# Performance work log

Measured on AMD Instinct MI355X. Metric: run time of the kernel, lower is better.

The kernel has to match this reference:

```python
import jax, jax.numpy as jnp
import numpy as np

TRUNC = (24, 24, 24)
OUT = (32, 32, 32)


def setup_inputs() -> dict:
    key = jax.random.key(0)
    x = jax.random.normal(key, (8, 32, 48, 48, 48), dtype=jnp.float32)
    return {"x": x}


def reference(x):
    # "DCT" as implemented in the source: real part of an ortho-normalized 3D FFT
    x_dct = jnp.real(jnp.fft.fftn(x, axes=(2, 3, 4), norm='ortho'))
    # crop to low-frequency corner, zero-pad up to output_size
    x_crop = x_dct[:, :, :TRUNC[0], :TRUNC[1], :TRUNC[2]]
    pad = ((0, 0), (0, 0),
           (0, OUT[0] - TRUNC[0]),
           (0, OUT[1] - TRUNC[1]),
           (0, OUT[2] - TRUNC[2]))
    x_pad = jnp.pad(x_crop, pad)
    # inverse transform on the output_size grid, keep real part
    x_idct = jnp.real(jnp.fft.ifftn(x_pad, axes=(2, 3, 4), norm='ortho'))
    return x_idct
```

## Files before the change

kernel.cpp:

```cpp
#include <hip/hip_runtime.h>
#include <math.h>


#define TWO_PI_48 0.13089969389957470f
#define TWO_PI_32 0.19634954084936207f
#define NORM_F    1.6611664e-05f

typedef _Float16 half8  __attribute__((ext_vector_type(8)));
typedef _Float16 half4v __attribute__((ext_vector_type(4)));
typedef float    f32x4  __attribute__((ext_vector_type(4)));

__device__ _Float16 T1frag[2][3][2][64][8];
__device__ _Float16 T2frag[2][3][2][64][8];
__device__ __align__(16) _Float16 TK2frag[2][4][3][64][8];
__device__ __align__(16) _Float16 MB2frag[2][4][2][64][8];
__device__ __align__(16) _Float16 TB3frag[2][2][2][64][8];

__device__ int g_twdone = 0;

__global__ void k_init_tw() {
  if (g_twdone) return;
  const int idx = blockIdx.x * 256 + threadIdx.x;
  if (idx < 3072) {
    const int j  = idx & 7;
    const int l  = (idx >> 3) & 63;
    const int ks = (idx >> 9) & 1;
    const int t  = idx >> 10;
    const int k  = ks * 32 + (l >> 4) * 8 + j;
    {
      const int m = t * 16 + (l & 15);
      float v = 0.f;
      if (k < 48) {
        const float a = (float)(((m % 24) * k) % 48) * TWO_PI_48;
        v = (m < 24) ? cosf(a) : -sinf(a);
      }
      const _Float16 h = (_Float16)v;
      T1frag[0][t][ks][l][j] = h;
      T1frag[1][t][ks][l][j] = (_Float16)(v - (float)h);
    }
    {
      const int c = t * 16 + (l & 15);
      float v = 0.f;
      if (k < 48) {
        const float a = (float)(((c % 24) * k) % 48) * TWO_PI_48;
        v = (c < 24) ? cosf(a) : sinf(a);
      }
      const _Float16 h = (_Float16)v;
      T2frag[0][t][ks][l][j] = h;
      T2frag[1][t][ks][l][j] = (_Float16)(v - (float)h);
    }
  } else if (idx < 3072 + 6144) {
    const int local = idx - 3072;
    const int j = local & 7, l = (local >> 3) & 63;
    const int rest = local >> 9;
    const int ks = rest % 3, mt = rest / 3;
    const int m   = mt * 16 + (l & 15);
    const int kap = ks * 32 + (l >> 4) * 8 + j;
    const int n1  = kap % 48;
    const bool isVi = kap >= 48;
    const int m1  = m & 31;
    const bool isWi = m >= 32;
    float acc = 0.f;
    for (int k1 = 0; k1 < 24; ++k1) {
      float s32v, c32v, s48v, c48v;
      sincosf((float)((k1 * m1) % 32) * TWO_PI_32, &s32v, &c32v);
      sincosf((float)((k1 * n1) % 48) * TWO_PI_48, &s48v, &c48v);
      acc = fmaf(isWi ? s32v : c32v, isVi ? s48v : c48v, acc);
    }
    const _Float16 h = (_Float16)acc;
    TK2frag[0][mt][ks][l][j] = h;
    TK2frag[1][mt][ks][l][j] = (_Float16)(acc - (float)h);
  } else if (idx < 3072 + 6144 + 4096) {
    const int local = idx - (3072 + 6144);
    const int j = local & 7, l = (local >> 3) & 63;
    const int rest = local >> 9;
    const int ks = rest & 1, mt = rest >> 1;
    const int m   = mt * 16 + (l & 15);
    const int kap = ks * 32 + (l >> 4) * 8 + j;
    float v = 0.f;
    if (kap < 48) {
      const int k2 = kap % 24;
      const int m2 = m & 31;
      float s, c;
      sincosf((float)((k2 * m2) % 32) * TWO_PI_32, &s, &c);
      if (m < 32) v = (kap < 24) ? c : -s;
      else        v = (kap < 24) ? s :  c;
    }
    const _Float16 h = (_Float16)v;
    MB2frag[0][mt][ks][l][j] = h;
    MB2frag[1][mt][ks][l][j] = (_Float16)(v - (float)h);
  } else if (idx < 15360) {
    const int local = idx - (3072 + 6144 + 4096);
    const int j = local & 7, l = (local >> 3) & 63;
    const int rest = local >> 9;
    const int ks = rest & 1, nt = rest >> 1;
    const int m3  = nt * 16 + (l & 15);
    const int kap = ks * 32 + (l >> 4) * 8 + j;
    float v = 0.f;
    if (kap < 48) {
      const int k3 = kap % 24;
      float s, c;
      sincosf((float)((k3 * m3) % 32) * TWO_PI_32, &s, &c);
      v = (kap < 24) ? c : -s;
    }
    const _Float16 h = (_Float16)v;
    TB3frag[0][nt][ks][l][j] = h;
    TB3frag[1][nt][ks][l][j] = (_Float16)(v - (float)h);
  }
}

__device__ inline void split8(const float* qf, half8& h, half8& lo) {
#pragma unroll
  for (int j = 0; j < 8; ++j) {
    const _Float16 hh = (_Float16)qf[j];
    h[j]  = hh;
    lo[j] = (_Float16)(qf[j] - (float)hh);
  }
}

__global__ __launch_bounds__(64) void k1_waveslab(const float* __restrict__ x,
                                                  float2* __restrict__ V) {
  const int n1   = blockIdx.x;
  const int bc   = blockIdx.y;
  const int lane = threadIdx.x;

  __shared__ __align__(16) unsigned char arena[13824];
  _Float16* Uh = (_Float16*)arena;
  _Float16* Ul = (_Float16*)(arena + 6912);
  float*    D2 = (float*)arena;

  const int c16  = lane & 15;
  const int kgrp = lane >> 4;
  const int kb   = kgrp * 8;

  const float* xs = x + (size_t)(bc * 48 + n1) * 2304;

  float4 xf[3][2][2];
  {
    const int k1i = 32 + kb;
#pragma unroll
    for (int nt = 0; nt < 3; ++nt) {
      const int c = nt * 16 + c16;
      const float4* p0 = (const float4*)(xs + c * 48 + kb);
      xf[nt][0][0] = p0[0]; xf[nt][0][1] = p0[1];
      if (k1i < 48) {
        const float4* p1 = (const float4*)(xs + c * 48 + k1i);
        xf[nt][1][0] = p1[0]; xf[nt][1][1] = p1[1];
      } else {
        xf[nt][1][0] = make_float4(0.f, 0.f, 0.f, 0.f);
        xf[nt][1][1] = make_float4(0.f, 0.f, 0.f, 0.f);
      }
    }
  }

  half8 t1h[3][2], t1l[3][2];
#pragma unroll
  for (int mt = 0; mt < 3; ++mt)
#pragma unroll
    for (int ks = 0; ks < 2; ++ks) {
      t1h[mt][ks] = *(const half8*)&T1frag[0][mt][ks][lane][0];
      t1l[mt][ks] = *(const half8*)&T1frag[1][mt][ks][lane][0];
    }

#pragma unroll
  for (int p = 0; p < 3; ++p) {
    const int i = lane + 64 * p;
    const int which = i / 48, r = i % 48;
    _Float16* base = (which & 2) ? Ul : Uh;
    *(half8*)&base[r * 72 + 48 + (which & 1) * 8] = (half8){};
  }

#pragma unroll
  for (int nt = 0; nt < 3; ++nt) {
    f32x4 acc0 = {}, acc1 = {}, acc2 = {};
#pragma unroll
    for (int ks = 0; ks < 2; ++ks) {
      const float4 qa = xf[nt][ks][0];
      const float4 qb = xf[nt][ks][1];
      const float qf[8] = {qa.x, qa.y, qa.z, qa.w, qb.x, qb.y, qb.z, qb.w};
      half8 bh, bl;
      split8(qf, bh, bl);
#pragma unroll
      for (int mt = 0; mt < 3; ++mt) {
        f32x4& acc = (mt == 0) ? acc0 : (mt == 1) ? acc1 : acc2;
        acc = __builtin_amdgcn_mfma_f32_16x16x32_f16(t1h[mt][ks], bh, acc, 0, 0, 0);
        acc = __builtin_amdgcn_mfma_f32_16x16x32_f16(t1h[mt][ks], bl, acc, 0, 0, 0);
        acc = __builtin_amdgcn_mfma_f32_16x16x32_f16(t1l[mt][ks], bh, acc, 0, 0, 0);
      }
    }

    {
      const int cc = nt * 16 + c16;
#pragma unroll
      for (int mt = 0; mt < 3; ++mt) {
        const int r0 = mt * 16 + kgrp * 4;
        const f32x4 acc = (mt == 0) ? acc0 : (mt == 1) ? acc1 : acc2;
#pragma unroll
        for (int r = 0; r < 4; ++r) {
          const float v = acc[r];
          const _Float16 h = (_Float16)v;
          Uh[(r0 + r) * 72 + cc] = h;
          Ul[(r0 + r) * 72 + cc] = (_Float16)(v - (float)h);
        }
      }
    }
  }

  half8 t2h[3][2], t2l[3][2];
#pragma unroll
  for (int mt = 0; mt < 3; ++mt)
#pragma unroll
    for (int ks = 0; ks < 2; ++ks) {
      t2h[mt][ks] = *(const half8*)&T2frag[0][mt][ks][lane][0];
      t2l[mt][ks] = *(const half8*)&T2frag[1][mt][ks][lane][0];
    }

  f32x4 a2[3][3] = {};
#pragma unroll
  for (int ks = 0; ks < 2; ++ks) {
#pragma unroll
    for (int mt = 0; mt < 3; ++mt) {
      const half8 ah = *(const half8*)&Uh[(mt * 16 + c16) * 72 + ks * 32 + kb];
      const half8 al = *(const half8*)&Ul[(mt * 16 + c16) * 72 + ks * 32 + kb];
#pragma unroll
      for (int nt2 = 0; nt2 < 3; ++nt2) {
        a2[mt][nt2] = __builtin_amdgcn_mfma_f32_16x16x32_f16(ah, t2h[nt2][ks], a2[mt][nt2], 0, 0, 0);
        a2[mt][nt2] = __builtin_amdgcn_mfma_f32_16x16x32_f16(ah, t2l[nt2][ks], a2[mt][nt2], 0, 0, 0);
        a2[mt][nt2] = __builtin_amdgcn_mfma_f32_16x16x32_f16(al, t2h[nt2][ks], a2[mt][nt2], 0, 0, 0);
      }
    }
  }

#pragma unroll
  for (int mt = 0; mt < 3; ++mt)
#pragma unroll
    for (int nt2 = 0; nt2 < 3; ++nt2) {
      const int r0 = mt * 16 + kgrp * 4;
      const int cc = nt2 * 16 + c16;
#pragma unroll
      for (int r = 0; r < 4; ++r)
        D2[(r0 + r) * 68 + cc] = a2[mt][nt2][r];
    }

#pragma unroll
  for (int q = 0; q < 9; ++q) {
    const int idx = lane + 64 * q;
    const int k3 = idx / 24, k2 = idx % 24;
    const float grr = D2[k3 * 68 + k2];
    const float gis = D2[(k3 + 24) * 68 + k2 + 24];
    const float gir = D2[(k3 + 24) * 68 + k2];
    const float grs = D2[k3 * 68 + k2 + 24];
    V[(size_t)bc * 27648 + (size_t)k3 * 1152 + n1 * 24 + k2] =
        make_float2(grr + gis, gir - grs);
  }
}

__global__ __launch_bounds__(192) void k2_mfma(const float2* __restrict__ V,
                                               float2* __restrict__ W) {
  const int k3   = blockIdx.x;
  const int byy  = blockIdx.y;
  const int tid  = threadIdx.x;
  const int lane = tid & 63;
  const int w    = tid >> 6;

  __shared__ __align__(16) float Bb[48 * 100];

  half8 kth[4][3], ktl[4][3];
#pragma unroll
  for (int mt = 0; mt < 4; ++mt)
#pragma unroll
    for (int ks = 0; ks < 3; ++ks) {
      kth[mt][ks] = *(const half8*)&TK2frag[0][mt][ks][lane][0];
      ktl[mt][ks] = *(const half8*)&TK2frag[1][mt][ks][lane][0];
    }

  const int kbase = (lane >> 4) * 8;
  const int c16   = lane & 15;
  const int cc    = w * 16 + c16;
  const int sE    = cc / 24, k2E = cc % 24;
  const int rbase = (lane >> 4) * 4;

  float4 vr[6];
  {
    const float4* g0 = (const float4*)(V + ((size_t)((byy * 4 + 0) * 24 + k3)) * 1152);
    const float4* g1 = (const float4*)(V + ((size_t)((byy * 4 + 1) * 24 + k3)) * 1152);
#pragma unroll
    for (int jj = 0; jj < 6; ++jj)
      vr[jj] = (jj < 3 ? g0 : g1)[tid + 192 * (jj % 3)];
  }

  for (int g = 0; g < 2; ++g) {
    const int bcp = byy * 2 + g;

    if (g) __syncthreads();

#pragma unroll
    for (int jj = 0; jj < 6; ++jj) {
      const int s = jj / 3;
      const int r = tid + 192 * (jj % 3);
      const int n1 = r / 12, c4 = r % 12;
      const float4 f = vr[jj];
      float* bp = &Bb[(s * 24 + c4 * 2) * 100 + n1];
      bp[0]   = f.x;  bp[48]  = f.y;
      bp[100] = f.z;  bp[148] = f.w;
    }
    if (g < 1) {
      const float4* g0 = (const float4*)(V + ((size_t)((bcp * 2 + 2) * 24 + k3)) * 1152);
      const float4* g1 = (const float4*)(V + ((size_t)((bcp * 2 + 3) * 24 + k3)) * 1152);
#pragma unroll
      for (int jj = 0; jj < 6; ++jj)
        vr[jj] = (jj < 3 ? g0 : g1)[tid + 192 * (jj % 3)];
    }
    __syncthreads();

    f32x4 a0 = {}, a1 = {}, a2 = {}, a3 = {};
#pragma unroll
    for (int ks = 0; ks < 3; ++ks) {
      const float4 q0 = *(const float4*)&Bb[cc * 100 + ks * 32 + kbase];
      const float4 q1 = *(const float4*)&Bb[cc * 100 + ks * 32 + kbase + 4];
      const float qf[8] = {q0.x, q0.y, q0.z, q0.w, q1.x, q1.y, q1.z, q1.w};
      half8 bh, bl;
      split8(qf, bh, bl);
#pragma unroll
      for (int mt = 0; mt < 4; ++mt) {
        f32x4& acc = (mt == 0) ? a0 : (mt == 1) ? a1 : (mt == 2) ? a2 : a3;
        acc = __builtin_amdgcn_mfma_f32_16x16x32_f16(kth[mt][ks], bh, acc, 0, 0, 0);
        acc = __builtin_amdgcn_mfma_f32_16x16x32_f16(kth[mt][ks], bl, acc, 0, 0, 0);
        acc = __builtin_amdgcn_mfma_f32_16x16x32_f16(ktl[mt][ks], bh, acc, 0, 0, 0);
      }
    }

    const int bc = bcp * 2 + sE;
    float2* wp = W + (size_t)bc * 18432 + (size_t)k3 * 24 + k2E;
#pragma unroll
    for (int mt = 0; mt < 2; ++mt) {
      const f32x4 wr = (mt == 0) ? a0 : a1;
      const f32x4 wi = (mt == 0) ? a2 : a3;
#pragma unroll
      for (int r = 0; r < 4; ++r) {
        const int m1 = mt * 16 + rbase + r;
        wp[(size_t)m1 * 576] = make_float2(wr[r], wi[r]);
      }
    }
  }
}

__global__ __launch_bounds__(128) void k3_mfma(const float2* __restrict__ W,
                                               float* __restrict__ out) {
  const int m1   = blockIdx.x;
  const int byy  = blockIdx.y;
  const int tid  = threadIdx.x;
  const int lane = tid & 63;
  const int w    = tid >> 6;

  __shared__ __align__(16) float Bt[32 * 68];
  __shared__ __align__(16) float Zb[32 * 68];

  half8 mbh[4][2], mbl[4][2];
#pragma unroll
  for (int mt = 0; mt < 4; ++mt)
#pragma unroll
    for (int ks = 0; ks < 2; ++ks) {
      mbh[mt][ks] = *(const half8*)&MB2frag[0][mt][ks][lane][0];
      mbl[mt][ks] = *(const half8*)&MB2frag[1][mt][ks][lane][0];
    }
  half8 tb3h[2], tb3l[2];
#pragma unroll
  for (int ks = 0; ks < 2; ++ks) {
    tb3h[ks] = *(const half8*)&TB3frag[0][w][ks][lane][0];
    tb3l[ks] = *(const half8*)&TB3frag[1][w][ks][lane][0];
  }

  for (int i = tid; i < 8 * 68; i += 128)  Bt[(24 + i / 68) * 68 + (i % 68)] = 0.f;
  for (int i = tid; i < 24 * 20; i += 128) Bt[(i / 20) * 68 + 48 + (i % 20)] = 0.f;
  for (int i = tid; i < 32 * 20; i += 128) Zb[(i / 20) * 68 + 48 + (i % 20)] = 0.f;

  const int kbase = (lane >> 4) * 8;
  const int c16   = lane & 15;
  const int cc    = w * 16 + c16;
  const int rbase = (lane >> 4) * 4;

  float4 vr0, vr1, vr2;
  {
    const float4* g4 = (const float4*)(W + (size_t)(byy * 2) * 18432 + (size_t)m1 * 576);
    vr0 = g4[tid];
    vr1 = g4[tid + 128];
    if (tid < 32) vr2 = g4[tid + 256];
  }

  for (int g = 0; g < 2; ++g) {
    const int bc = byy * 2 + g;

    {
      const float4 fr[3] = {vr0, vr1, vr2};
#pragma unroll
      for (int jj = 0; jj < 3; ++jj) {
        const int i4 = tid + 128 * jj;
        if (jj < 2 || tid < 32) {
          const int k3 = i4 / 12, c4 = i4 % 12;
          const float4 f = fr[jj];
          Bt[k3 * 68 + 2 * c4]          = f.x;
          Bt[k3 * 68 + 24 + 2 * c4]     = f.y;
          Bt[k3 * 68 + 2 * c4 + 1]      = f.z;
          Bt[k3 * 68 + 24 + 2 * c4 + 1] = f.w;
        }
      }
    }
    if (g < 1) {
      const float4* g4 = (const float4*)(W + (size_t)(bc + 1) * 18432 + (size_t)m1 * 576);
      vr0 = g4[tid];
      vr1 = g4[tid + 128];
      if (tid < 32) vr2 = g4[tid + 256];
    }
    __syncthreads();

    f32x4 z0 = {}, z1 = {}, z2 = {}, z3 = {};
#pragma unroll
    for (int ks = 0; ks < 2; ++ks) {
      const float4 q0 = *(const float4*)&Bt[cc * 68 + ks * 32 + kbase];
      const float4 q1 = *(const float4*)&Bt[cc * 68 + ks * 32 + kbase + 4];
      const float qf[8] = {q0.x, q0.y, q0.z, q0.w, q1.x, q1.y, q1.z, q1.w};
      half8 bh, bl;
      split8(qf, bh, bl);
#pragma unroll
      for (int mt = 0; mt < 4; ++mt) {
        f32x4& acc = (mt == 0) ? z0 : (mt == 1) ? z1 : (mt == 2) ? z2 : z3;
        acc = __builtin_amdgcn_mfma_f32_16x16x32_f16(mbh[mt][ks], bh, acc, 0, 0, 0);
        acc = __builtin_amdgcn_mfma_f32_16x16x32_f16(mbh[mt][ks], bl, acc, 0, 0, 0);
        acc = __builtin_amdgcn_mfma_f32_16x16x32_f16(mbl[mt][ks], bh, acc, 0, 0, 0);
      }
    }
    if (cc < 24) {
#pragma unroll
      for (int mt = 0; mt < 4; ++mt) {
        const f32x4 acc = (mt == 0) ? z0 : (mt == 1) ? z1 : (mt == 2) ? z2 : z3;
        const int row0 = mt * 16 + rbase;
#pragma unroll
        for (int r = 0; r < 4; ++r) {
          const int row = row0 + r;
          if (row < 32) Zb[row * 68 + cc]              = acc[r];
          else          Zb[(row - 32) * 68 + 24 + cc]  = acc[r];
        }
      }
    }
    __syncthreads();

    f32x4 o0 = {}, o1 = {};
#pragma unroll
    for (int ks = 0; ks < 2; ++ks) {
#pragma unroll
      for (int mt = 0; mt < 2; ++mt) {
        const float4 q0 = *(const float4*)&Zb[(mt * 16 + c16) * 68 + ks * 32 + kbase];
        const float4 q1 = *(const float4*)&Zb[(mt * 16 + c16) * 68 + ks * 32 + kbase + 4];
        const float qf[8] = {q0.x, q0.y, q0.z, q0.w, q1.x, q1.y, q1.z, q1.w};
        half8 ah, al;
        split8(qf, ah, al);
        f32x4& acc = (mt == 0) ? o0 : o1;
        acc = __builtin_amdgcn_mfma_f32_16x16x32_f16(ah, tb3h[ks], acc, 0, 0, 0);
        acc = __builtin_amdgcn_mfma_f32_16x16x32_f16(ah, tb3l[ks], acc, 0, 0, 0);
        acc = __builtin_amdgcn_mfma_f32_16x16x32_f16(al, tb3h[ks], acc, 0, 0, 0);
      }
    }
    float* op = out + (size_t)(bc * 32 + m1) * 1024;
#pragma unroll
    for (int mt = 0; mt < 2; ++mt) {
      const f32x4 acc = (mt == 0) ? o0 : o1;
#pragma unroll
      for (int r = 0; r < 4; ++r) {
        const int m2 = mt * 16 + rbase + r;
        op[m2 * 32 + cc] = acc[r] * NORM_F;
      }
    }
  }

  if (tid == 0 && blockIdx.x == 0 && blockIdx.y == 0) g_twdone = 1;
}

extern "C" void kernel_launch(void* const* d_in, const int* in_sizes, int n_in,
                              void* d_out, int out_size, void* d_ws, size_t ws_size,
                              hipStream_t stream) {
  const float* x = (const float*)d_in[0];
  float* out = (float*)d_out;
  float2* V = (float2*)d_ws;
  float2* W = (float2*)((char*)d_ws + 56623104);

  k_init_tw   <<<dim3(60), dim3(256), 0, stream>>>();
  k1_waveslab <<<dim3(48, 256), dim3(64), 0, stream>>>(x, V);
  k2_mfma     <<<dim3(24, 64), dim3(192), 0, stream>>>(V, W);
  k3_mfma     <<<dim3(32, 128), dim3(128), 0, stream>>>(W, out);
}
```

Before: 81.44 us.

## Process six slabs per k1 block with register double-buffered prefetch

Each k1 wavefront now handles six consecutive n1 slabs instead of one. Both twiddle fragment sets are loaded once per block and reused across all six slabs. The input for the next slab is prefetched into a second register buffer while the current slab's second-stage MFMAs and stores run. The goal is to amortise twiddle loads and launch overhead and to hide global load latency, at the cost of more registers (launch_bounds set to 2 blocks) and fewer blocks (2048 instead of 12288).

```diff
diff --git a/kernel.cpp b/kernel.cpp
--- a/kernel.cpp
+++ b/kernel.cpp
@@ -118,9 +118,26 @@
   }
 }
 
-__global__ __launch_bounds__(64) void k1_waveslab(const float* __restrict__ x,
-                                                  float2* __restrict__ V) {
-  const int n1   = blockIdx.x;
+__device__ inline void load_xf(const float* xs, int c16, int kb, float4 f[3][2][2]) {
+  const int k1i = 32 + kb;
+#pragma unroll
+  for (int nt = 0; nt < 3; ++nt) {
+    const int c = nt * 16 + c16;
+    const float4* p0 = (const float4*)(xs + c * 48 + kb);
+    f[nt][0][0] = p0[0]; f[nt][0][1] = p0[1];
+    if (k1i < 48) {
+      const float4* p1 = (const float4*)(xs + c * 48 + k1i);
+      f[nt][1][0] = p1[0]; f[nt][1][1] = p1[1];
+    } else {
+      f[nt][1][0] = make_float4(0.f, 0.f, 0.f, 0.f);
+      f[nt][1][1] = make_float4(0.f, 0.f, 0.f, 0.f);
+    }
+  }
+}
+
+__global__ __launch_bounds__(64, 2) void k1_waveslab(const float* __restrict__ x,
+                                                     float2* __restrict__ V) {
+  const int bx   = blockIdx.x;
   const int bc   = blockIdx.y;
   const int lane = threadIdx.x;
 
@@ -133,33 +150,20 @@
   const int kgrp = lane >> 4;
   const int kb   = kgrp * 8;
 
-  const float* xs = x + (size_t)(bc * 48 + n1) * 2304;
-
-  float4 xf[3][2][2];
-  {
-    const int k1i = 32 + kb;
-#pragma unroll
-    for (int nt = 0; nt < 3; ++nt) {
-      const int c = nt * 16 + c16;
-      const float4* p0 = (const float4*)(xs + c * 48 + kb);
-      xf[nt][0][0] = p0[0]; xf[nt][0][1] = p0[1];
-      if (k1i < 48) {
-        const float4* p1 = (const float4*)(xs + c * 48 + k1i);
-        xf[nt][1][0] = p1[0]; xf[nt][1][1] = p1[1];
-      } else {
-        xf[nt][1][0] = make_float4(0.f, 0.f, 0.f, 0.f);
-        xf[nt][1][1] = make_float4(0.f, 0.f, 0.f, 0.f);
-      }
-    }
-  }
-
-  half8 t1h[3][2], t1l[3][2];
+  const float* xc = x + (size_t)(bc * 48) * 2304;
+
+  float4 xfA[3][2][2], xfB[3][2][2];
+  load_xf(xc + (size_t)(bx * 6) * 2304, c16, kb, xfA);
+
+  half8 t1h[3][2], t1l[3][2], t2h[3][2], t2l[3][2];
 #pragma unroll
   for (int mt = 0; mt < 3; ++mt)
 #pragma unroll
     for (int ks = 0; ks < 2; ++ks) {
       t1h[mt][ks] = *(const half8*)&T1frag[0][mt][ks][lane][0];
       t1l[mt][ks] = *(const half8*)&T1frag[1][mt][ks][lane][0];
+      t2h[mt][ks] = *(const half8*)&T2frag[0][mt][ks][lane][0];
+      t2l[mt][ks] = *(const half8*)&T2frag[1][mt][ks][lane][0];
     }
 
 #pragma unroll
@@ -171,87 +175,96 @@
   }
 
 #pragma unroll
-  for (int nt = 0; nt < 3; ++nt) {
-    f32x4 acc0 = {}, acc1 = {}, acc2 = {};
+  for (int it = 0; it < 6; ++it) {
+    const int n1 = bx * 6 + it;
+    float4 (&cur)[3][2][2] = (it & 1) ? xfB : xfA;
+    float4 (&nxt)[3][2][2] = (it & 1) ? xfA : xfB;
+
+#pragma unroll
+    for (int nt = 0; nt < 3; ++nt) {
+      f32x4 acc0 = {}, acc1 = {}, acc2 = {};
+#pragma unroll
+      for (int ks = 0; ks < 2; ++ks) {
+        const float4 qa = cur[nt][ks][0];
+        const float4 qb = cur[nt][ks][1];
+        const float qf[8] = {qa.x, qa.y, qa.z, qa.w, qb.x, qb.y, qb.z, qb.w};
+        half8 bh, bl;
+        split8(qf, bh, bl);
+#pragma unroll
+        for (int mt = 0; mt < 3; ++mt) {
+          f32x4& acc = (mt == 0) ? acc0 : (mt == 1) ? acc1 : acc2;
+          acc = __builtin_amdgcn_mfma_f32_16x16x32_f16(t1h[mt][ks], bh, acc, 0, 0, 0);
+          acc = __builtin_amdgcn_mfma_f32_16x16x32_f16(t1h[mt][ks], bl, acc, 0, 0, 0);
+          acc = __builtin_amdgcn_mfma_f32_16x16x32_f16(t1l[mt][ks], bh, acc, 0, 0, 0);
+        }
+      }
+      {
+        const int cc = nt * 16 + c16;
+#pragma unroll
+        for (int mt = 0; mt < 3; ++mt) {
+          const int r0 = mt * 16 + kgrp * 4;
+          const f32x4 acc = (mt == 0) ? acc0 : (mt == 1) ? acc1 : acc2;
+#pragma unroll
+          for (int r = 0; r < 4; ++r) {
+            const float v = acc[r];
+            const _Float16 h = (_Float16)v;
+            Uh[(r0 + r) * 72 + cc] = h;
+            Ul[(r0 + r) * 72 + cc] = (_Float16)(v - (float)h);
+          }
+        }
+      }
+    }
+
+    if (it < 5) load_xf(xc + (size_t)(n1 + 1) * 2304, c16, kb, nxt);
+
+    f32x4 a2[3][3] = {};
 #pragma unroll
     for (int ks = 0; ks < 2; ++ks) {
-      const float4 qa = xf[nt][ks][0];
-      const float4 qb = xf[nt][ks][1];
-      const float qf[8] = {qa.x, qa.y, qa.z, qa.w, qb.x, qb.y, qb.z, qb.w};
-      half8 bh, bl;
-      split8(qf, bh, bl);
 #pragma unroll
       for (int mt = 0; mt < 3; ++mt) {
-        f32x4& acc = (mt == 0) ? acc0 : (mt == 1) ? acc1 : acc2;
-        acc = __builtin_amdgcn_mfma_f32_16x16x32_f16(t1h[mt][ks], bh, acc, 0, 0, 0);
-        acc = __builtin_amdgcn_mfma_f32_16x16x32_f16(t1h[mt][ks], bl, acc, 0, 0, 0);
-        acc = __builtin_amdgcn_mfma_f32_16x16x32_f16(t1l[mt][ks], bh, acc, 0, 0, 0);
-      }
-    }
-
-    {
-      const int cc = nt * 16 + c16;
-#pragma unroll
-      for (int mt = 0; mt < 3; ++mt) {
+        const half8 ah = *(const half8*)&Uh[(mt * 16 + c16) * 72 + ks * 32 + kb];
+        const half8 al = *(const half8*)&Ul[(mt * 16 + c16) * 72 + ks * 32 + kb];
+#pragma unroll
+        for (int nt2 = 0; nt2 < 3; ++nt2) {
+          a2[mt][nt2] = __builtin_amdgcn_mfma_f32_16x16x32_f16(ah, t2h[nt2][ks], a2[mt][nt2], 0, 0, 0);
+          a2[mt][nt2] = __builtin_amdgcn_mfma_f32_16x16x32_f16(ah, t2l[nt2][ks], a2[mt][nt2], 0, 0, 0);
+          a2[mt][nt2] = __builtin_amdgcn_mfma_f32_16x16x32_f16(al, t2h[nt2][ks], a2[mt][nt2], 0, 0, 0);
+        }
+      }
+    }
+
+#pragma unroll
+    for (int mt = 0; mt < 3; ++mt)
+#pragma unroll
+      for (int nt2 = 0; nt2 < 3; ++nt2) {
         const int r0 = mt * 16 + kgrp * 4;
-        const f32x4 acc = (mt == 0) ? acc0 : (mt == 1) ? acc1 : acc2;
-#pragma unroll
-        for (int r = 0; r < 4; ++r) {
-          const float v = acc[r];
-          const _Float16 h = (_Float16)v;
-          Uh[(r0 + r) * 72 + cc] = h;
-          Ul[(r0 + r) * 72 + cc] = (_Float16)(v - (float)h);
-        }
-      }
-    }
-  }
-
-  half8 t2h[3][2], t2l[3][2];
-#pragma unroll
-  for (int mt = 0; mt < 3; ++mt)
-#pragma unroll
-    for (int ks = 0; ks < 2; ++ks) {
-      t2h[mt][ks] = *(const half8*)&T2frag[0][mt][ks][lane][0];
-      t2l[mt][ks] = *(const half8*)&T2frag[1][mt][ks][lane][0];
-    }
-
-  f32x4 a2[3][3] = {};
-#pragma unroll
-  for (int ks = 0; ks < 2; ++ks) {
-#pragma unroll
-    for (int mt = 0; mt < 3; ++mt) {
-      const half8 ah = *(const half8*)&Uh[(mt * 16 + c16) * 72 + ks * 32 + kb];
-      const half8 al = *(const half8*)&Ul[(mt * 16 + c16) * 72 + ks * 32 + kb];
-#pragma unroll
-      for (int nt2 = 0; nt2 < 3; ++nt2) {
-        a2[mt][nt2] = __builtin_amdgcn_mfma_f32_16x16x32_f16(ah, t2h[nt2][ks], a2[mt][nt2], 0, 0, 0);
-        a2[mt][nt2] = __builtin_amdgcn_mfma_f32_16x16x32_f16(ah, t2l[nt2][ks], a2[mt][nt2], 0, 0, 0);
-        a2[mt][nt2] = __builtin_amdgcn_mfma_f32_16x16x32_f16(al, t2h[nt2][ks], a2[mt][nt2], 0, 0, 0);
-      }
-    }
-  }
-
-#pragma unroll
-  for (int mt = 0; mt < 3; ++mt)
-#pragma unroll
-    for (int nt2 = 0; nt2 < 3; ++nt2) {
-      const int r0 = mt * 16 + kgrp * 4;
-      const int cc = nt2 * 16 + c16;
-#pragma unroll
-      for (int r = 0; r < 4; ++r)
-        D2[(r0 + r) * 68 + cc] = a2[mt][nt2][r];
-    }
-
-#pragma unroll
-  for (int q = 0; q < 9; ++q) {
-    const int idx = lane + 64 * q;
-    const int k3 = idx / 24, k2 = idx % 24;
-    const float grr = D2[k3 * 68 + k2];
-    const float gis = D2[(k3 + 24) * 68 + k2 + 24];
-    const float gir = D2[(k3 + 24) * 68 + k2];
-    const float grs = D2[k3 * 68 + k2 + 24];
-    V[(size_t)bc * 27648 + (size_t)k3 * 1152 + n1 * 24 + k2] =
-        make_float2(grr + gis, gir - grs);
+        const int cc = nt2 * 16 + c16;
+#pragma unroll
+        for (int r = 0; r < 4; ++r)
+          D2[(r0 + r) * 68 + cc] = a2[mt][nt2][r];
+      }
+
+#pragma unroll
+    for (int q = 0; q < 9; ++q) {
+      const int idx = lane + 64 * q;
+      const int k3 = idx / 24, k2 = idx % 24;
+      const float grr = D2[k3 * 68 + k2];
+      const float gis = D2[(k3 + 24) * 68 + k2 + 24];
+      const float gir = D2[(k3 + 24) * 68 + k2];
+      const float grs = D2[k3 * 68 + k2 + 24];
+      V[(size_t)bc * 27648 + (size_t)k3 * 1152 + n1 * 24 + k2] =
+          make_float2(grr + gis, gir - grs);
+    }
+
+    if (it < 5) {
+#pragma unroll
+      for (int p = 0; p < 3; ++p) {
+        const int i = lane + 64 * p;
+        const int which = i / 48, r = i % 48;
+        _Float16* base = (which & 2) ? Ul : Uh;
+        *(half8*)&base[r * 72 + 48 + (which & 1) * 8] = (half8){};
+      }
+    }
   }
 }
 
@@ -485,7 +498,7 @@
   float2* W = (float2*)((char*)d_ws + 56623104);
 
   k_init_tw   <<<dim3(60), dim3(256), 0, stream>>>();
-  k1_waveslab <<<dim3(48, 256), dim3(64), 0, stream>>>(x, V);
+  k1_waveslab <<<dim3(8, 256), dim3(64), 0, stream>>>(x, V);
   k2_mfma     <<<dim3(24, 64), dim3(192), 0, stream>>>(V, W);
   k3_mfma     <<<dim3(32, 128), dim3(128), 0, stream>>>(W, out);
 }
```

After: 81.15 us. Within noise of the previous version (-0.4%).
